# Kernel optimization log

Measured on AMD Instinct MI355X. Metric: run time of the kernel, lower is better.

The kernel has to match this reference:

```python
import jax, jax.numpy as jnp
import numpy as np

B, T, D = 1024, 512, 64   # batch, seq_len, input_dim
H, L, OUT = 8, 3, 1       # hidden (mid_dim), num_layers, output_dim


def setup_inputs() -> dict:
    key = jax.random.key(0)
    ks = jax.random.split(key, 18)
    s = 1.0 / np.sqrt(H)  # torch LSTM default init scale
    u = lambda k, shape: jax.random.uniform(k, shape, jnp.float32, -s, s)
    return {
        "input_seq": jax.random.normal(ks[0], (B, T, D), jnp.float32),
        "h0": jax.random.normal(ks[1], (L, B, H), jnp.float32),
        "c0": jax.random.normal(ks[2], (L, B, H), jnp.float32),
        # encoder LSTM params (layer0 input dim differs)
        "enc_Wih0": u(ks[3], (4 * H, D)),
        "enc_Wih_rest": u(ks[4], (L - 1, 4 * H, H)),
        "enc_Whh": u(ks[5], (L, 4 * H, H)),
        "enc_bih": u(ks[6], (L, 4 * H)),
        "enc_bhh": u(ks[7], (L, 4 * H)),
        # decoder LSTM params
        "dec_Wih0": u(ks[8], (4 * H, D)),
        "dec_Wih_rest": u(ks[9], (L - 1, 4 * H, H)),
        "dec_Whh": u(ks[10], (L, 4 * H, H)),
        "dec_bih": u(ks[11], (L, 4 * H)),
        "dec_bhh": u(ks[12], (L, 4 * H)),
        # decoder output projection
        "lin_W": u(ks[13], (OUT, H)),
        "lin_b": u(ks[14], (OUT,)),
    }


def _cell(x, h, c, Wih, Whh, b):
    # one LSTM cell step, torch gate order: i, f, g, o
    gates = x @ Wih.T + h @ Whh.T + b  # [B, 4H]
    i, f, g, o = jnp.split(gates, 4, axis=-1)
    c2 = jax.nn.sigmoid(f) * c + jax.nn.sigmoid(i) * jnp.tanh(g)
    h2 = jax.nn.sigmoid(o) * jnp.tanh(c2)
    return h2, c2


def _stack_step(h, c, x_t, Wih0, Wih_rest, Whh, bih, bhh):
    # one timestep through all L layers; h, c: [L, B, H]
    hs, cs = [], []
    inp = x_t
    for l in range(L):
        Wih = Wih0 if l == 0 else Wih_rest[l - 1]
        h_l, c_l = _cell(inp, h[l], c[l], Wih, Whh[l], bih[l] + bhh[l])
        hs.append(h_l)
        cs.append(c_l)
        inp = h_l
    return jnp.stack(hs), jnp.stack(cs)


def reference(input_seq, h0, c0, enc_Wih0, enc_Wih_rest, enc_Whh, enc_bih, enc_bhh,
              dec_Wih0, dec_Wih_rest, dec_Whh, dec_bih, dec_bhh, lin_W, lin_b):
    x_tbd = jnp.transpose(input_seq, (1, 0, 2))  # [T, B, D] for scan

    # Encoder: full-sequence 3-layer LSTM, keep final (h, c)
    def enc_step(carry, x_t):
        h, c = carry
        h2, c2 = _stack_step(h, c, x_t, enc_Wih0, enc_Wih_rest, enc_Whh, enc_bih, enc_bhh)
        return (h2, c2), None

    (h, c), _ = jax.lax.scan(enc_step, (h0, c0), x_tbd)

    # Decoder: one LSTM step per timestep, fed the input at that step
    def dec_step(carry, x_t):
        h, c = carry
        h2, c2 = _stack_step(h, c, x_t, dec_Wih0, dec_Wih_rest, dec_Whh, dec_bih, dec_bhh)
        return (h2, c2), None

    (h, c), _ = jax.lax.scan(dec_step, (h, c), x_tbd)

    # original returns outputs[:, -1, :] = linear applied to last decoder output
    pred_last = h[-1] @ lin_W.T + lin_b  # [B, OUT]
    return pred_last
```

## Files before the change

### kernel.cpp

```cpp
#include <hip/hip_runtime.h>

#define TT 512
#define DD 64
#define BB 1024
#define PF 8
#define HH 8

typedef float v2f __attribute__((ext_vector_type(2)));

__device__ __forceinline__ float fexp2(float x){ return __builtin_amdgcn_exp2f(x); }
__device__ __forceinline__ float frcp (float x){ return __builtin_amdgcn_rcpf(x); }

__device__ __forceinline__ v2f bc2(float s){ v2f r; r.x = s; r.y = s; return r; }

#if defined(__has_builtin)
#if __has_builtin(__builtin_elementwise_fma)
#define HAVE_EW_FMA 1
#endif
#endif

__device__ __forceinline__ v2f vfma(v2f a, v2f b, v2f c){
#ifdef HAVE_EW_FMA
  return __builtin_elementwise_fma(a, b, c);
#else
  v2f r; r.x = fmaf(a.x, b.x, c.x); r.y = fmaf(a.y, b.y, c.y); return r;
#endif
}

template<int C>
__device__ __forceinline__ float dppf(float x){
  return __int_as_float(__builtin_amdgcn_update_dpp(0, __float_as_int(x), C, 0xF, 0xF, true));
}
template<int C>
__device__ __forceinline__ int dppi(int x){
  return __builtin_amdgcn_update_dpp(0, x, C, 0xF, 0xF, true);
}

template<int N> struct IC { static constexpr int v = N; };

__global__ __launch_bounds__(256) void proj_kernel(
    const float* __restrict__ x,
    const float* __restrict__ eWih0, const float* __restrict__ eBih, const float* __restrict__ eBhh,
    const float* __restrict__ dWih0, const float* __restrict__ dBih, const float* __restrict__ dBhh,
    float* __restrict__ P)
{
  __shared__ __align__(16) float xs[4][2][16 * 64];
  const int tid  = threadIdx.x;
  const int w    = tid >> 6;
  const int lane = tid & 63;
  const int ph   = lane >> 5;
  const int r    = lane & 31;
  const float* W = ph ? dWih0 : eWih0;
  const float b0 = ph ? (dBih[r] + dBhh[r]) : (eBih[r] + eBhh[r]);
  const int gate = r >> 3, j = r & 7;
  const int pos  = (gate * 4 + (j & 3)) * 2 + (j >> 2);

  float Wx[64];
#pragma unroll
  for (int k = 0; k < 16; ++k) {
    float4 wq = *(const float4*)(W + r * 64 + k * 4);
    Wx[k*4+0] = wq.x; Wx[k*4+1] = wq.y; Wx[k*4+2] = wq.z; Wx[k*4+3] = wq.w;
  }

  const int base_row = (blockIdx.x * 4 + w) * 64;
  const float* xg = x + (size_t)base_row * 64;

  float4 st[4];
#pragma unroll
  for (int i = 0; i < 4; ++i) st[i] = *(const float4*)(xg + i * 256 + lane * 4);
#pragma unroll
  for (int i = 0; i < 4; ++i) *(float4*)&xs[w][0][i * 256 + lane * 4] = st[i];
#pragma unroll
  for (int i = 0; i < 4; ++i) st[i] = *(const float4*)(xg + 1024 + i * 256 + lane * 4);

#pragma unroll 1
  for (int g = 0; g < 4; ++g) {
    const float* buf = &xs[w][g & 1][0];
#pragma unroll 2
    for (int ri = 0; ri < 16; ++ri) {
      float a0 = b0, a1 = 0.f, a2 = 0.f, a3 = 0.f;
#pragma unroll
      for (int kc = 0; kc < 16; ++kc) {
        float4 xv = *(const float4*)(buf + ri * 64 + kc * 4);
        a0 = fmaf(Wx[kc*4+0], xv.x, a0);
        a1 = fmaf(Wx[kc*4+1], xv.y, a1);
        a2 = fmaf(Wx[kc*4+2], xv.z, a2);
        a3 = fmaf(Wx[kc*4+3], xv.w, a3);
      }
      const int row = base_row + g * 16 + ri;
      const int e = row >> 9, t = row & 511;
      P[((size_t)((ph << 10) + e) * TT + t) * 32 + pos] = (a0 + a1) + (a2 + a3);
    }
    if (g < 3) {
#pragma unroll
      for (int i = 0; i < 4; ++i) *(float4*)&xs[w][(g + 1) & 1][i * 256 + lane * 4] = st[i];
      if (g < 2) {
#pragma unroll
        for (int i = 0; i < 4; ++i)
          st[i] = *(const float4*)(xg + (size_t)(g + 2) * 1024 + i * 256 + lane * 4);
      }
    }
  }
}

__global__ __launch_bounds__(64) void recur_kernel(
    const float* __restrict__ P,
    const float* __restrict__ h0,    const float* __restrict__ c0,
    const float* __restrict__ eWihR, const float* __restrict__ eWhh,
    const float* __restrict__ eBih,  const float* __restrict__ eBhh,
    const float* __restrict__ dWihR, const float* __restrict__ dWhh,
    const float* __restrict__ dBih,  const float* __restrict__ dBhh,
    const float* __restrict__ linW,  const float* __restrict__ linB,
    float* __restrict__ out)
{
  const int lane = threadIdx.x;
  const int row  = lane >> 4;
  const int L    = lane & 15;
  const int u    = L >> 2;
  const int g    = L & 3;
  const int e    = blockIdx.x * 4 + row;

  const bool is_tanh = (g == 2);
  const float ns_act = is_tanh ? -2.885390082f : -1.44269504f;
  const float a_act  = is_tanh ? 2.0f : 1.0f;
  const float b_act  = is_tanh ? -1.0f : 0.0f;

  const int p4 = dppi<0x124>(u);
  const int d  = __builtin_amdgcn_readfirstlane((p4 - u) & 3);

  v2f H[3], cs[3], sd[3];
  v2f bd1 = bc2(0.f), bd2 = bc2(0.f);
  v2f WS[3][8], WB[2][8], Bss[2];

#pragma unroll
  for (int l = 0; l < 3; ++l) {
    H[l].x  = h0[((size_t)l * BB + e) * HH + u];
    H[l].y  = h0[((size_t)l * BB + e) * HH + u + 4];
    cs[l].x = c0[((size_t)l * BB + e) * HH + u];
    cs[l].y = c0[((size_t)l * BB + e) * HH + u + 4];
  }

  auto load_phase = [&](const float* WihR, const float* Whh,
                        const float* Bih, const float* Bhh) {
#pragma unroll
    for (int l = 0; l < 3; ++l) {
      const int r0 = l * 32 + g * 8 + u;
#pragma unroll
      for (int k = 0; k < 4; ++k) {
        const int col = (u + d * k) & 3;
        WS[l][k].x     = Whh[r0 * 8 + col];
        WS[l][k].y     = Whh[(r0 + 4) * 8 + col];
        WS[l][4 + k].x = Whh[r0 * 8 + 4 + col];
        WS[l][4 + k].y = Whh[(r0 + 4) * 8 + 4 + col];
      }
    }
#pragma unroll
    for (int l = 0; l < 2; ++l) {
      const int r0 = l * 32 + g * 8 + u;
#pragma unroll
      for (int k = 0; k < 4; ++k) {
        const int col = (u + d * k) & 3;
        WB[l][k].x     = WihR[r0 * 8 + col];
        WB[l][k].y     = WihR[(r0 + 4) * 8 + col];
        WB[l][4 + k].x = WihR[r0 * 8 + 4 + col];
        WB[l][4 + k].y = WihR[(r0 + 4) * 8 + 4 + col];
      }
      Bss[l].x = Bih[(l + 1) * 32 + g * 8 + u]     + Bhh[(l + 1) * 32 + g * 8 + u];
      Bss[l].y = Bih[(l + 1) * 32 + g * 8 + u + 4] + Bhh[(l + 1) * 32 + g * 8 + u + 4];
    }
#pragma unroll
    for (int l = 0; l < 3; ++l) {
      float A0[4], B0[4];
      A0[0] = H[l].x; A0[1] = dppf<0x124>(H[l].x); A0[2] = dppf<0x128>(H[l].x); A0[3] = dppf<0x12C>(H[l].x);
      B0[0] = H[l].y; B0[1] = dppf<0x124>(H[l].y); B0[2] = dppf<0x128>(H[l].y); B0[3] = dppf<0x12C>(H[l].y);
      v2f acc = bc2(0.f);
      if (l) acc = Bss[l - 1];
#pragma unroll
      for (int k = 0; k < 4; ++k) {
        acc = vfma(WS[l][k],     bc2(A0[k]), acc);
        acc = vfma(WS[l][4 + k], bc2(B0[k]), acc);
      }
      sd[l] = acc;
    }
  };

  auto lstep = [&](auto LC, v2f in) -> v2f {
    constexpr int l = decltype(LC)::v;
    v2f pre = in + sd[l];
    v2f ex; ex.x = fexp2(ns_act * pre.x); ex.y = fexp2(ns_act * pre.y);
    v2f rc; rc.x = frcp(1.f + ex.x);      rc.y = frcp(1.f + ex.y);
    v2f act = vfma(bc2(a_act), rc, bc2(b_act));
    v2f Gi, Gf, Gg, Go;
    Gi.x = dppf<0x00>(act.x); Gi.y = dppf<0x00>(act.y);
    Gf.x = dppf<0x55>(act.x); Gf.y = dppf<0x55>(act.y);
    Gg.x = dppf<0xAA>(act.x); Gg.y = dppf<0xAA>(act.y);
    Go.x = dppf<0xFF>(act.x); Go.y = dppf<0xFF>(act.y);
    v2f cn = vfma(Gf, cs[l], Gi * Gg);
    cs[l] = cn;
    v2f tx; tx.x = fexp2(-2.885390082f * cn.x); tx.y = fexp2(-2.885390082f * cn.y);
    v2f tr; tr.x = frcp(1.f + tx.x);            tr.y = frcp(1.f + tx.y);
    v2f th = vfma(bc2(2.f), tr, bc2(-1.f));
    v2f hn = Go * th;
    H[l] = hn;
    float A0[4], B0[4];
    A0[0] = hn.x; A0[1] = dppf<0x124>(hn.x); A0[2] = dppf<0x128>(hn.x); A0[3] = dppf<0x12C>(hn.x);
    B0[0] = hn.y; B0[1] = dppf<0x124>(hn.y); B0[2] = dppf<0x128>(hn.y); B0[3] = dppf<0x12C>(hn.y);
    v2f accS;
    if constexpr (l > 0) accS = Bss[l - 1]; else accS = bc2(0.f);
    v2f accB = bc2(0.f);
#pragma unroll
    for (int k = 0; k < 4; ++k) {
      accS = vfma(WS[l][k],     bc2(A0[k]), accS);
      accS = vfma(WS[l][4 + k], bc2(B0[k]), accS);
      if constexpr (l < 2) {
        accB = vfma(WB[l][k],     bc2(A0[k]), accB);
        accB = vfma(WB[l][4 + k], bc2(B0[k]), accB);
      }
    }
    sd[l] = accS;
    return accB;
  };

#pragma unroll 1
  for (int ph = 0; ph < 2; ++ph) {
    if (ph == 0) load_phase(eWihR, eWhh, eBih, eBhh);
    else         load_phase(dWihR, dWhh, dBih, dBhh);

    const float* Pb = P + ((size_t)((ph << 10) + e) * TT) * 32 + (g * 4 + u) * 2;

    v2f pf[PF];
#pragma unroll
    for (int k = 0; k < PF; ++k) pf[k] = *(const v2f*)(Pb + k * 32);

#pragma unroll
    for (int k = 0; k < PF; ++k) {
      v2f cur = pf[k];
      pf[k] = *(const v2f*)(Pb + (k + PF) * 32);
      v2f n1 = lstep(IC<0>{}, cur);
      v2f n2 = bc2(0.f);
      if (k >= 1) n2 = lstep(IC<1>{}, bd1);
      if (k >= 2) (void)lstep(IC<2>{}, bd2);
      bd1 = n1; bd2 = n2;
    }

#pragma unroll 1
    for (int t = PF; t < TT; t += PF) {
#pragma unroll
      for (int k = 0; k < PF; ++k) {
        v2f cur = pf[k];
        int tn = t + k + PF; if (tn > TT - 1) tn = TT - 1;
        pf[k] = *(const v2f*)(Pb + tn * 32);
        v2f n1 = lstep(IC<0>{}, cur);
        v2f n2 = lstep(IC<1>{}, bd1);
        (void)lstep(IC<2>{}, bd2);
        bd1 = n1; bd2 = n2;
      }
    }

    v2f dd = lstep(IC<1>{}, bd1);
    (void)lstep(IC<2>{}, bd2);
    (void)lstep(IC<2>{}, dd);
  }

  float lwA[4], lwB[4];
#pragma unroll
  for (int k = 0; k < 4; ++k) {
    const int col = (u + d * k) & 3;
    lwA[k] = linW[col];
    lwB[k] = linW[4 + col];
  }
  float A0[4], B0[4];
  A0[0] = H[2].x; A0[1] = dppf<0x124>(H[2].x); A0[2] = dppf<0x128>(H[2].x); A0[3] = dppf<0x12C>(H[2].x);
  B0[0] = H[2].y; B0[1] = dppf<0x124>(H[2].y); B0[2] = dppf<0x128>(H[2].y); B0[3] = dppf<0x12C>(H[2].y);
  float pred = linB[0];
#pragma unroll
  for (int k = 0; k < 4; ++k) {
    pred = fmaf(lwA[k], A0[k], pred);
    pred = fmaf(lwB[k], B0[k], pred);
  }
  if (L == 0) out[e] = pred;
}

__global__ __launch_bounds__(64) void seq2seq_fallback(
    const float* __restrict__ x, const float* __restrict__ h0, const float* __restrict__ c0,
    const float* __restrict__ eWih0, const float* __restrict__ eWihR, const float* __restrict__ eWhh,
    const float* __restrict__ eBih,  const float* __restrict__ eBhh,
    const float* __restrict__ dWih0, const float* __restrict__ dWihR, const float* __restrict__ dWhh,
    const float* __restrict__ dBih,  const float* __restrict__ dBhh,
    const float* __restrict__ linW,  const float* __restrict__ linB, float* __restrict__ out)
{
  const int tid = threadIdx.x;
  const int g   = tid & 31;
  const int grp = tid & 32;
  const int jj  = g & 7;
  const int e   = blockIdx.x * 2 + (tid >> 5);
  const bool is_tanh = ((g >> 3) == 2);
  const float s_act = is_tanh ? 2.885390082f : 1.44269504f;
  const float a_act = is_tanh ? 2.0f : 1.0f;
  const float b_act = is_tanh ? -1.0f : 0.0f;
  float hrep[3][8]; float cc[3];
#pragma unroll
  for (int l = 0; l < 3; ++l) {
#pragma unroll
    for (int k = 0; k < 8; ++k) hrep[l][k] = h0[((size_t)l * BB + e) * HH + k];
    cc[l] = c0[((size_t)l * BB + e) * HH + jj];
  }
  for (int p = 0; p < 2; ++p) {
    const float* Wih0 = p ? dWih0 : eWih0;  const float* WihR = p ? dWihR : eWihR;
    const float* Whh  = p ? dWhh  : eWhh;   const float* Bih  = p ? dBih  : eBih;
    const float* Bhh  = p ? dBhh  : eBhh;
    float Wx[64];
#pragma unroll
    for (int k = 0; k < 64; k += 4) {
      float4 w = *(const float4*)(Wih0 + g * 64 + k);
      Wx[k] = w.x; Wx[k+1] = w.y; Wx[k+2] = w.z; Wx[k+3] = w.w;
    }
    float Wh[3][8], Wi[2][8], bias[3];
#pragma unroll
    for (int l = 0; l < 3; ++l) {
#pragma unroll
      for (int k = 0; k < 8; ++k) Wh[l][k] = Whh[(l*32+g)*8+k];
      bias[l] = Bih[l*32+g] + Bhh[l*32+g];
    }
#pragma unroll
    for (int l = 0; l < 2; ++l)
#pragma unroll
      for (int k = 0; k < 8; ++k) Wi[l][k] = WihR[(l*32+g)*8+k];
    const float* xrow = x + (size_t)e * TT * DD;
    for (int t = 0; t < TT; ++t) {
      float4 acc = make_float4(bias[0], 0.f, 0.f, 0.f);
#pragma unroll
      for (int kc = 0; kc < 16; ++kc) {
        float4 xv = *(const float4*)(xrow + kc * 4);
        acc.x = fmaf(Wx[kc*4+0], xv.x, acc.x); acc.y = fmaf(Wx[kc*4+1], xv.y, acc.y);
        acc.z = fmaf(Wx[kc*4+2], xv.z, acc.z); acc.w = fmaf(Wx[kc*4+3], xv.w, acc.w);
      }
      float pre = (acc.x + acc.y) + (acc.z + acc.w);
      { float r0=0.f,r1=0.f;
#pragma unroll
        for (int k = 0; k < 8; k += 2) { r0=fmaf(Wh[0][k],hrep[0][k],r0); r1=fmaf(Wh[0][k+1],hrep[0][k+1],r1); }
        pre += r0 + r1; }
#pragma unroll
      for (int l = 0; l < 3; ++l) {
        if (l > 0) {
          float r0 = bias[l], r1 = 0.f;
#pragma unroll
          for (int k = 0; k < 8; k += 2) {
            r0=fmaf(Wi[l-1][k],hrep[l-1][k],r0); r1=fmaf(Wi[l-1][k+1],hrep[l-1][k+1],r1);
            r0=fmaf(Wh[l][k],hrep[l][k],r0);     r1=fmaf(Wh[l][k+1],hrep[l][k+1],r1);
          }
          pre = r0 + r1;
        }
        float act = fmaf(a_act, frcp(1.0f + fexp2(-s_act * pre)), b_act);
        float iv = __shfl(act, grp + jj);
        float fv = __shfl(act, grp + 8 + jj);
        float gv = __shfl(act, grp + 16 + jj);
        float ov = __shfl(act, grp + 24 + jj);
        float cn = fmaf(fv, cc[l], iv * gv);
        cc[l] = cn;
        float th = fmaf(2.0f, frcp(1.0f + fexp2(-2.885390082f * cn)), -1.0f);
        float hn = ov * th;
#pragma unroll
        for (int k = 0; k < 8; ++k) hrep[l][k] = __shfl(hn, grp + k);
      }
      xrow += DD;
    }
  }
  float pred = linB[0];
#pragma unroll
  for (int k = 0; k < 8; ++k) pred = fmaf(linW[k], hrep[2][k], pred);
  if (g == 0) out[e] = pred;
}

extern "C" void kernel_launch(void* const* d_in, const int* in_sizes, int n_in,
                              void* d_out, int out_size, void* d_ws, size_t ws_size,
                              hipStream_t stream) {
  const float* x     = (const float*)d_in[0];
  const float* h0    = (const float*)d_in[1];
  const float* c0    = (const float*)d_in[2];
  const float* eWih0 = (const float*)d_in[3];
  const float* eWihR = (const float*)d_in[4];
  const float* eWhh  = (const float*)d_in[5];
  const float* eBih  = (const float*)d_in[6];
  const float* eBhh  = (const float*)d_in[7];
  const float* dWih0 = (const float*)d_in[8];
  const float* dWihR = (const float*)d_in[9];
  const float* dWhh  = (const float*)d_in[10];
  const float* dBih  = (const float*)d_in[11];
  const float* dBhh  = (const float*)d_in[12];
  const float* linW  = (const float*)d_in[13];
  const float* linB  = (const float*)d_in[14];
  float* out = (float*)d_out;

  const size_t P_BYTES = (size_t)2 * BB * TT * 32 * sizeof(float);
  if (ws_size >= P_BYTES) {
    float* P = (float*)d_ws;
    proj_kernel<<<2048, 256, 0, stream>>>(x, eWih0, eBih, eBhh, dWih0, dBih, dBhh, P);
    recur_kernel<<<BB / 4, 64, 0, stream>>>(P, h0, c0, eWihR, eWhh, eBih, eBhh,
                                            dWihR, dWhh, dBih, dBhh, linW, linB, out);
  } else {
    seq2seq_fallback<<<BB / 2, 64, 0, stream>>>(x, h0, c0, eWih0, eWihR, eWhh, eBih, eBhh,
                                                dWih0, dWihR, dWhh, dBih, dBhh, linW, linB, out);
  }
}
```

Baseline: 644.8 us.

## Split LSTM layers across three wavefronts with LDS handoff pipeline

```diff
diff --git a/kernel.cpp b/kernel.cpp
--- a/kernel.cpp
+++ b/kernel.cpp
@@ -35,8 +35,6 @@
 __device__ __forceinline__ int dppi(int x){
   return __builtin_amdgcn_update_dpp(0, x, C, 0xF, 0xF, true);
 }
-
-template<int N> struct IC { static constexpr int v = N; };
 
 __global__ __launch_bounds__(256) void proj_kernel(
     const float* __restrict__ x,
@@ -103,7 +101,7 @@
   }
 }
 
-__global__ __launch_bounds__(64) void recur_kernel(
+__global__ __launch_bounds__(192) void recur_kernel(
     const float* __restrict__ P,
     const float* __restrict__ h0,    const float* __restrict__ c0,
     const float* __restrict__ eWihR, const float* __restrict__ eWhh,
@@ -113,7 +111,12 @@
     const float* __restrict__ linW,  const float* __restrict__ linB,
     float* __restrict__ out)
 {
-  const int lane = threadIdx.x;
+  __shared__ v2f bufA[2][64];
+  __shared__ v2f bufB[2][64];
+
+  const int tid  = threadIdx.x;
+  const int w    = tid >> 6;
+  const int lane = tid & 63;
   const int row  = lane >> 4;
   const int L    = lane & 15;
   const int u    = L >> 2;
@@ -125,68 +128,59 @@
   const float a_act  = is_tanh ? 2.0f : 1.0f;
   const float b_act  = is_tanh ? -1.0f : 0.0f;
 
+  const bool seedb = (w > 0);
+  const bool below = (w < 2);
+
   const int p4 = dppi<0x124>(u);
   const int d  = __builtin_amdgcn_readfirstlane((p4 - u) & 3);
 
-  v2f H[3], cs[3], sd[3];
-  v2f bd1 = bc2(0.f), bd2 = bc2(0.f);
-  v2f WS[3][8], WB[2][8], Bss[2];
-
-#pragma unroll
-  for (int l = 0; l < 3; ++l) {
-    H[l].x  = h0[((size_t)l * BB + e) * HH + u];
-    H[l].y  = h0[((size_t)l * BB + e) * HH + u + 4];
-    cs[l].x = c0[((size_t)l * BB + e) * HH + u];
-    cs[l].y = c0[((size_t)l * BB + e) * HH + u + 4];
-  }
+  v2f Hm, cm, sdm;
+  v2f WSm[8], WBm[8], Bsm = bc2(0.f);
+
+  Hm.x = h0[((size_t)w * BB + e) * HH + u];
+  Hm.y = h0[((size_t)w * BB + e) * HH + u + 4];
+  cm.x = c0[((size_t)w * BB + e) * HH + u];
+  cm.y = c0[((size_t)w * BB + e) * HH + u + 4];
 
   auto load_phase = [&](const float* WihR, const float* Whh,
                         const float* Bih, const float* Bhh) {
-#pragma unroll
-    for (int l = 0; l < 3; ++l) {
-      const int r0 = l * 32 + g * 8 + u;
+    const int r0 = w * 32 + g * 8 + u;
+#pragma unroll
+    for (int k = 0; k < 4; ++k) {
+      const int col = (u + d * k) & 3;
+      WSm[k].x     = Whh[r0 * 8 + col];
+      WSm[k].y     = Whh[(r0 + 4) * 8 + col];
+      WSm[4 + k].x = Whh[r0 * 8 + 4 + col];
+      WSm[4 + k].y = Whh[(r0 + 4) * 8 + 4 + col];
+    }
+    if (below) {
 #pragma unroll
       for (int k = 0; k < 4; ++k) {
         const int col = (u + d * k) & 3;
-        WS[l][k].x     = Whh[r0 * 8 + col];
-        WS[l][k].y     = Whh[(r0 + 4) * 8 + col];
-        WS[l][4 + k].x = Whh[r0 * 8 + 4 + col];
-        WS[l][4 + k].y = Whh[(r0 + 4) * 8 + 4 + col];
-      }
-    }
-#pragma unroll
-    for (int l = 0; l < 2; ++l) {
-      const int r0 = l * 32 + g * 8 + u;
-#pragma unroll
-      for (int k = 0; k < 4; ++k) {
-        const int col = (u + d * k) & 3;
-        WB[l][k].x     = WihR[r0 * 8 + col];
-        WB[l][k].y     = WihR[(r0 + 4) * 8 + col];
-        WB[l][4 + k].x = WihR[r0 * 8 + 4 + col];
-        WB[l][4 + k].y = WihR[(r0 + 4) * 8 + 4 + col];
-      }
-      Bss[l].x = Bih[(l + 1) * 32 + g * 8 + u]     + Bhh[(l + 1) * 32 + g * 8 + u];
-      Bss[l].y = Bih[(l + 1) * 32 + g * 8 + u + 4] + Bhh[(l + 1) * 32 + g * 8 + u + 4];
-    }
-#pragma unroll
-    for (int l = 0; l < 3; ++l) {
-      float A0[4], B0[4];
-      A0[0] = H[l].x; A0[1] = dppf<0x124>(H[l].x); A0[2] = dppf<0x128>(H[l].x); A0[3] = dppf<0x12C>(H[l].x);
-      B0[0] = H[l].y; B0[1] = dppf<0x124>(H[l].y); B0[2] = dppf<0x128>(H[l].y); B0[3] = dppf<0x12C>(H[l].y);
-      v2f acc = bc2(0.f);
-      if (l) acc = Bss[l - 1];
-#pragma unroll
-      for (int k = 0; k < 4; ++k) {
-        acc = vfma(WS[l][k],     bc2(A0[k]), acc);
-        acc = vfma(WS[l][4 + k], bc2(B0[k]), acc);
-      }
-      sd[l] = acc;
-    }
+        WBm[k].x     = WihR[r0 * 8 + col];
+        WBm[k].y     = WihR[(r0 + 4) * 8 + col];
+        WBm[4 + k].x = WihR[r0 * 8 + 4 + col];
+        WBm[4 + k].y = WihR[(r0 + 4) * 8 + 4 + col];
+      }
+    }
+    if (seedb) {
+      Bsm.x = Bih[w * 32 + g * 8 + u]     + Bhh[w * 32 + g * 8 + u];
+      Bsm.y = Bih[w * 32 + g * 8 + u + 4] + Bhh[w * 32 + g * 8 + u + 4];
+    }
+    float A0[4], B0[4];
+    A0[0] = Hm.x; A0[1] = dppf<0x124>(Hm.x); A0[2] = dppf<0x128>(Hm.x); A0[3] = dppf<0x12C>(Hm.x);
+    B0[0] = Hm.y; B0[1] = dppf<0x124>(Hm.y); B0[2] = dppf<0x128>(Hm.y); B0[3] = dppf<0x12C>(Hm.y);
+    v2f acc = seedb ? Bsm : bc2(0.f);
+#pragma unroll
+    for (int k = 0; k < 4; ++k) {
+      acc = vfma(WSm[k],     bc2(A0[k]), acc);
+      acc = vfma(WSm[4 + k], bc2(B0[k]), acc);
+    }
+    sdm = acc;
   };
 
-  auto lstep = [&](auto LC, v2f in) -> v2f {
-    constexpr int l = decltype(LC)::v;
-    v2f pre = in + sd[l];
+  auto lstep = [&](v2f in) -> v2f {
+    v2f pre = in + sdm;
     v2f ex; ex.x = fexp2(ns_act * pre.x); ex.y = fexp2(ns_act * pre.y);
     v2f rc; rc.x = frcp(1.f + ex.x);      rc.y = frcp(1.f + ex.y);
     v2f act = vfma(bc2(a_act), rc, bc2(b_act));
@@ -195,29 +189,31 @@
     Gf.x = dppf<0x55>(act.x); Gf.y = dppf<0x55>(act.y);
     Gg.x = dppf<0xAA>(act.x); Gg.y = dppf<0xAA>(act.y);
     Go.x = dppf<0xFF>(act.x); Go.y = dppf<0xFF>(act.y);
-    v2f cn = vfma(Gf, cs[l], Gi * Gg);
-    cs[l] = cn;
+    v2f cn = vfma(Gf, cm, Gi * Gg);
+    cm = cn;
     v2f tx; tx.x = fexp2(-2.885390082f * cn.x); tx.y = fexp2(-2.885390082f * cn.y);
     v2f tr; tr.x = frcp(1.f + tx.x);            tr.y = frcp(1.f + tx.y);
     v2f th = vfma(bc2(2.f), tr, bc2(-1.f));
     v2f hn = Go * th;
-    H[l] = hn;
+    Hm = hn;
     float A0[4], B0[4];
     A0[0] = hn.x; A0[1] = dppf<0x124>(hn.x); A0[2] = dppf<0x128>(hn.x); A0[3] = dppf<0x12C>(hn.x);
     B0[0] = hn.y; B0[1] = dppf<0x124>(hn.y); B0[2] = dppf<0x128>(hn.y); B0[3] = dppf<0x12C>(hn.y);
-    v2f accS;
-    if constexpr (l > 0) accS = Bss[l - 1]; else accS = bc2(0.f);
+    v2f accS = seedb ? Bsm : bc2(0.f);
+#pragma unroll
+    for (int k = 0; k < 4; ++k) {
+      accS = vfma(WSm[k],     bc2(A0[k]), accS);
+      accS = vfma(WSm[4 + k], bc2(B0[k]), accS);
+    }
+    sdm = accS;
     v2f accB = bc2(0.f);
-#pragma unroll
-    for (int k = 0; k < 4; ++k) {
-      accS = vfma(WS[l][k],     bc2(A0[k]), accS);
-      accS = vfma(WS[l][4 + k], bc2(B0[k]), accS);
-      if constexpr (l < 2) {
-        accB = vfma(WB[l][k],     bc2(A0[k]), accB);
-        accB = vfma(WB[l][4 + k], bc2(B0[k]), accB);
-      }
-    }
-    sd[l] = accS;
+    if (below) {
+#pragma unroll
+      for (int k = 0; k < 4; ++k) {
+        accB = vfma(WBm[k],     bc2(A0[k]), accB);
+        accB = vfma(WBm[4 + k], bc2(B0[k]), accB);
+      }
+    }
     return accB;
   };
 
@@ -229,56 +225,72 @@
     const float* Pb = P + ((size_t)((ph << 10) + e) * TT) * 32 + (g * 4 + u) * 2;
 
     v2f pf[PF];
-#pragma unroll
-    for (int k = 0; k < PF; ++k) pf[k] = *(const v2f*)(Pb + k * 32);
-
-#pragma unroll
-    for (int k = 0; k < PF; ++k) {
-      v2f cur = pf[k];
-      pf[k] = *(const v2f*)(Pb + (k + PF) * 32);
-      v2f n1 = lstep(IC<0>{}, cur);
-      v2f n2 = bc2(0.f);
-      if (k >= 1) n2 = lstep(IC<1>{}, bd1);
-      if (k >= 2) (void)lstep(IC<2>{}, bd2);
-      bd1 = n1; bd2 = n2;
+    if (w == 0) {
+#pragma unroll
+      for (int k = 0; k < PF; ++k) pf[k] = *(const v2f*)(Pb + k * 32);
     }
 
 #pragma unroll 1
-    for (int t = PF; t < TT; t += PF) {
-#pragma unroll
-      for (int k = 0; k < PF; ++k) {
-        v2f cur = pf[k];
-        int tn = t + k + PF; if (tn > TT - 1) tn = TT - 1;
-        pf[k] = *(const v2f*)(Pb + tn * 32);
-        v2f n1 = lstep(IC<0>{}, cur);
-        v2f n2 = lstep(IC<1>{}, bd1);
-        (void)lstep(IC<2>{}, bd2);
-        bd1 = n1; bd2 = n2;
-      }
-    }
-
-    v2f dd = lstep(IC<1>{}, bd1);
-    (void)lstep(IC<2>{}, bd2);
-    (void)lstep(IC<2>{}, dd);
-  }
-
-  float lwA[4], lwB[4];
-#pragma unroll
-  for (int k = 0; k < 4; ++k) {
-    const int col = (u + d * k) & 3;
-    lwA[k] = linW[col];
-    lwB[k] = linW[4 + col];
-  }
-  float A0[4], B0[4];
-  A0[0] = H[2].x; A0[1] = dppf<0x124>(H[2].x); A0[2] = dppf<0x128>(H[2].x); A0[3] = dppf<0x12C>(H[2].x);
-  B0[0] = H[2].y; B0[1] = dppf<0x124>(H[2].y); B0[2] = dppf<0x128>(H[2].y); B0[3] = dppf<0x12C>(H[2].y);
-  float pred = linB[0];
-#pragma unroll
-  for (int k = 0; k < 4; ++k) {
-    pred = fmaf(lwA[k], A0[k], pred);
-    pred = fmaf(lwB[k], B0[k], pred);
-  }
-  if (L == 0) out[e] = pred;
+    for (int kb = 0; kb < TT; kb += PF) {
+#pragma unroll
+      for (int j = 0; j < PF; ++j) {
+        const int k = kb + j;
+        if (w == 0) {
+          v2f cur = pf[j];
+          int tn = k + PF; if (tn > TT - 1) tn = TT - 1;
+          pf[j] = *(const v2f*)(Pb + tn * 32);
+          v2f n1 = lstep(cur);
+          bufA[j & 1][lane] = n1;
+        } else if (w == 1) {
+          if (k >= 1) {
+            v2f i1 = bufA[(j ^ 1) & 1][lane];
+            v2f n2 = lstep(i1);
+            bufB[(j ^ 1) & 1][lane] = n2;
+          }
+        } else {
+          if (k >= 2) {
+            v2f i2 = bufB[j & 1][lane];
+            (void)lstep(i2);
+          }
+        }
+        __syncthreads();
+      }
+    }
+    if (w == 1) {
+      v2f i1 = bufA[1][lane];
+      v2f n2 = lstep(i1);
+      bufB[1][lane] = n2;
+    } else if (w == 2) {
+      v2f i2 = bufB[0][lane];
+      (void)lstep(i2);
+    }
+    __syncthreads();
+    if (w == 2) {
+      v2f i2 = bufB[1][lane];
+      (void)lstep(i2);
+    }
+    __syncthreads();
+  }
+
+  if (w == 2) {
+    float lwA[4], lwB[4];
+#pragma unroll
+    for (int k = 0; k < 4; ++k) {
+      const int col = (u + d * k) & 3;
+      lwA[k] = linW[col];
+      lwB[k] = linW[4 + col];
+    }
+    float A0[4], B0[4];
+    A0[0] = Hm.x; A0[1] = dppf<0x124>(Hm.x); A0[2] = dppf<0x128>(Hm.x); A0[3] = dppf<0x12C>(Hm.x);
+    B0[0] = Hm.y; B0[1] = dppf<0x124>(Hm.y); B0[2] = dppf<0x128>(Hm.y); B0[3] = dppf<0x12C>(Hm.y);
+    float pred = linB[0];
+#pragma unroll
+    for (int k = 0; k < 4; ++k) {
+      pred = fmaf(lwA[k], A0[k], pred);
+      pred = fmaf(lwB[k], B0[k], pred);
+    }
+    if (L == 0) out[e] = pred;
+  }
 }
 
 __global__ __launch_bounds__(64) void seq2seq_fallback(
@@ -396,8 +408,8 @@
   if (ws_size >= P_BYTES) {
     float* P = (float*)d_ws;
     proj_kernel<<<2048, 256, 0, stream>>>(x, eWih0, eBih, eBhh, dWih0, dBih, dBhh, P);
-    recur_kernel<<<BB / 4, 64, 0, stream>>>(P, h0, c0, eWihR, eWhh, eBih, eBhh,
-                                            dWihR, dWhh, dBih, dBhh, linW, linB, out);
+    recur_kernel<<<BB / 4, 192, 0, stream>>>(P, h0, c0, eWihR, eWhh, eBih, eBhh,
+                                             dWihR, dWhh, dBih, dBhh, linW, linB, out);
   } else {
     seq2seq_fallback<<<BB / 2, 64, 0, stream>>>(x, h0, c0, eWih0, eWihR, eWhh, eBih, eBhh,
                                                 dWih0, dWihR, dWhh, dBih, dBhh, linW, linB, out);
```

New measurement: 651.8 us. No clear change (+1.1%).

## Spread recurrence over 32 lanes per sequence, one hidden unit per lane

Applied to the files above, without the earlier changes.

```diff
diff --git a/kernel.cpp b/kernel.cpp
--- a/kernel.cpp
+++ b/kernel.cpp
@@ -11,22 +11,6 @@
 __device__ __forceinline__ float fexp2(float x){ return __builtin_amdgcn_exp2f(x); }
 __device__ __forceinline__ float frcp (float x){ return __builtin_amdgcn_rcpf(x); }
 
-__device__ __forceinline__ v2f bc2(float s){ v2f r; r.x = s; r.y = s; return r; }
-
-#if defined(__has_builtin)
-#if __has_builtin(__builtin_elementwise_fma)
-#define HAVE_EW_FMA 1
-#endif
-#endif
-
-__device__ __forceinline__ v2f vfma(v2f a, v2f b, v2f c){
-#ifdef HAVE_EW_FMA
-  return __builtin_elementwise_fma(a, b, c);
-#else
-  v2f r; r.x = fmaf(a.x, b.x, c.x); r.y = fmaf(a.y, b.y, c.y); return r;
-#endif
-}
-
 template<int C>
 __device__ __forceinline__ float dppf(float x){
   return __int_as_float(__builtin_amdgcn_update_dpp(0, __float_as_int(x), C, 0xF, 0xF, true));
@@ -34,6 +18,10 @@
 template<int C>
 __device__ __forceinline__ int dppi(int x){
   return __builtin_amdgcn_update_dpp(0, x, C, 0xF, 0xF, true);
+}
+
+__device__ __forceinline__ float swz16(float x){
+  return __int_as_float(__builtin_amdgcn_ds_swizzle(__float_as_int(x), 0x401F));
 }
 
 template<int N> struct IC { static constexpr int v = N; };
@@ -103,7 +91,7 @@
   }
 }
 
-__global__ __launch_bounds__(64) void recur_kernel(
+__global__ __launch_bounds__(128) void recur_kernel(
     const float* __restrict__ P,
     const float* __restrict__ h0,    const float* __restrict__ c0,
     const float* __restrict__ eWihR, const float* __restrict__ eWhh,
@@ -113,111 +101,113 @@
     const float* __restrict__ linW,  const float* __restrict__ linB,
     float* __restrict__ out)
 {
-  const int lane = threadIdx.x;
-  const int row  = lane >> 4;
-  const int L    = lane & 15;
-  const int u    = L >> 2;
-  const int g    = L & 3;
-  const int e    = blockIdx.x * 4 + row;
+  const int tid = threadIdx.x;
+  const int idx = tid & 31;
+  const int v   = idx >> 2;
+  const int g   = idx & 3;
+  const int b   = v & 3;
+  const bool rB = (v >= 4);
+  const int e   = blockIdx.x * 4 + (tid >> 5);
 
   const bool is_tanh = (g == 2);
   const float ns_act = is_tanh ? -2.885390082f : -1.44269504f;
   const float a_act  = is_tanh ? 2.0f : 1.0f;
   const float b_act  = is_tanh ? -1.0f : 0.0f;
 
-  const int p4 = dppi<0x124>(u);
-  const int d  = __builtin_amdgcn_readfirstlane((p4 - u) & 3);
-
-  v2f H[3], cs[3], sd[3];
-  v2f bd1 = bc2(0.f), bd2 = bc2(0.f);
-  v2f WS[3][8], WB[2][8], Bss[2];
+  const int qidx = (tid >> 2) & 3;
+  const int p4 = dppi<0x124>(qidx);
+  const int d  = __builtin_amdgcn_readfirstlane((p4 - qidx) & 3);
+
+  float H[3], cs[3], sd[3];
+  float bd1 = 0.f, bd2 = 0.f;
+  float WS[3][8], WB[2][8], Bss[2];
 
 #pragma unroll
   for (int l = 0; l < 3; ++l) {
-    H[l].x  = h0[((size_t)l * BB + e) * HH + u];
-    H[l].y  = h0[((size_t)l * BB + e) * HH + u + 4];
-    cs[l].x = c0[((size_t)l * BB + e) * HH + u];
-    cs[l].y = c0[((size_t)l * BB + e) * HH + u + 4];
-  }
+    H[l]  = h0[((size_t)l * BB + e) * HH + v];
+    cs[l] = c0[((size_t)l * BB + e) * HH + v];
+  }
+
+  auto bcast = [&](float hn, float* A, float* Bv) {
+    float Hsw = swz16(hn);
+    float Lo = rB ? Hsw : hn;
+    float Hi = rB ? hn : Hsw;
+    A[0]  = Lo; A[1]  = dppf<0x124>(Lo); A[2]  = dppf<0x128>(Lo); A[3]  = dppf<0x12C>(Lo);
+    Bv[0] = Hi; Bv[1] = dppf<0x124>(Hi); Bv[2] = dppf<0x128>(Hi); Bv[3] = dppf<0x12C>(Hi);
+  };
 
   auto load_phase = [&](const float* WihR, const float* Whh,
                         const float* Bih, const float* Bhh) {
 #pragma unroll
     for (int l = 0; l < 3; ++l) {
-      const int r0 = l * 32 + g * 8 + u;
+      const int r0 = l * 32 + g * 8 + v;
 #pragma unroll
       for (int k = 0; k < 4; ++k) {
-        const int col = (u + d * k) & 3;
-        WS[l][k].x     = Whh[r0 * 8 + col];
-        WS[l][k].y     = Whh[(r0 + 4) * 8 + col];
-        WS[l][4 + k].x = Whh[r0 * 8 + 4 + col];
-        WS[l][4 + k].y = Whh[(r0 + 4) * 8 + 4 + col];
+        const int col = (b + d * k) & 3;
+        WS[l][k]     = Whh[r0 * 8 + col];
+        WS[l][4 + k] = Whh[r0 * 8 + 4 + col];
       }
     }
 #pragma unroll
     for (int l = 0; l < 2; ++l) {
-      const int r0 = l * 32 + g * 8 + u;
+      const int r0 = l * 32 + g * 8 + v;
 #pragma unroll
       for (int k = 0; k < 4; ++k) {
-        const int col = (u + d * k) & 3;
-        WB[l][k].x     = WihR[r0 * 8 + col];
-        WB[l][k].y     = WihR[(r0 + 4) * 8 + col];
-        WB[l][4 + k].x = WihR[r0 * 8 + 4 + col];
-        WB[l][4 + k].y = WihR[(r0 + 4) * 8 + 4 + col];
-      }
-      Bss[l].x = Bih[(l + 1) * 32 + g * 8 + u]     + Bhh[(l + 1) * 32 + g * 8 + u];
-      Bss[l].y = Bih[(l + 1) * 32 + g * 8 + u + 4] + Bhh[(l + 1) * 32 + g * 8 + u + 4];
+        const int col = (b + d * k) & 3;
+        WB[l][k]     = WihR[r0 * 8 + col];
+        WB[l][4 + k] = WihR[r0 * 8 + 4 + col];
+      }
+      Bss[l] = Bih[(l + 1) * 32 + g * 8 + v] + Bhh[(l + 1) * 32 + g * 8 + v];
     }
 #pragma unroll
     for (int l = 0; l < 3; ++l) {
-      float A0[4], B0[4];
-      A0[0] = H[l].x; A0[1] = dppf<0x124>(H[l].x); A0[2] = dppf<0x128>(H[l].x); A0[3] = dppf<0x12C>(H[l].x);
-      B0[0] = H[l].y; B0[1] = dppf<0x124>(H[l].y); B0[2] = dppf<0x128>(H[l].y); B0[3] = dppf<0x12C>(H[l].y);
-      v2f acc = bc2(0.f);
-      if (l) acc = Bss[l - 1];
+      float A[4], Bv[4];
+      bcast(H[l], A, Bv);
+      float acc = l ? Bss[l - 1] : 0.f;
 #pragma unroll
       for (int k = 0; k < 4; ++k) {
-        acc = vfma(WS[l][k],     bc2(A0[k]), acc);
-        acc = vfma(WS[l][4 + k], bc2(B0[k]), acc);
+        acc = fmaf(WS[l][k],     A[k],  acc);
+        acc = fmaf(WS[l][4 + k], Bv[k], acc);
       }
       sd[l] = acc;
     }
   };
 
-  auto lstep = [&](auto LC, v2f in) -> v2f {
+  auto lstep = [&](auto LC, float in) -> float {
     constexpr int l = decltype(LC)::v;
-    v2f pre = in + sd[l];
-    v2f ex; ex.x = fexp2(ns_act * pre.x); ex.y = fexp2(ns_act * pre.y);
-    v2f rc; rc.x = frcp(1.f + ex.x);      rc.y = frcp(1.f + ex.y);
-    v2f act = vfma(bc2(a_act), rc, bc2(b_act));
-    v2f Gi, Gf, Gg, Go;
-    Gi.x = dppf<0x00>(act.x); Gi.y = dppf<0x00>(act.y);
-    Gf.x = dppf<0x55>(act.x); Gf.y = dppf<0x55>(act.y);
-    Gg.x = dppf<0xAA>(act.x); Gg.y = dppf<0xAA>(act.y);
-    Go.x = dppf<0xFF>(act.x); Go.y = dppf<0xFF>(act.y);
-    v2f cn = vfma(Gf, cs[l], Gi * Gg);
+    float pre = in + sd[l];
+    float ex  = fexp2(ns_act * pre);
+    float rc  = frcp(1.f + ex);
+    float act = fmaf(a_act, rc, b_act);
+    float Gi = dppf<0x00>(act);
+    float Gf = dppf<0x55>(act);
+    float Gg = dppf<0xAA>(act);
+    float Go = dppf<0xFF>(act);
+    float cn = fmaf(Gf, cs[l], Gi * Gg);
     cs[l] = cn;
-    v2f tx; tx.x = fexp2(-2.885390082f * cn.x); tx.y = fexp2(-2.885390082f * cn.y);
-    v2f tr; tr.x = frcp(1.f + tx.x);            tr.y = frcp(1.f + tx.y);
-    v2f th = vfma(bc2(2.f), tr, bc2(-1.f));
-    v2f hn = Go * th;
+    float tx = fexp2(-2.885390082f * cn);
+    float tr = frcp(1.f + tx);
+    float th = fmaf(2.f, tr, -1.f);
+    float hn = Go * th;
     H[l] = hn;
-    float A0[4], B0[4];
-    A0[0] = hn.x; A0[1] = dppf<0x124>(hn.x); A0[2] = dppf<0x128>(hn.x); A0[3] = dppf<0x12C>(hn.x);
-    B0[0] = hn.y; B0[1] = dppf<0x124>(hn.y); B0[2] = dppf<0x128>(hn.y); B0[3] = dppf<0x12C>(hn.y);
-    v2f accS;
-    if constexpr (l > 0) accS = Bss[l - 1]; else accS = bc2(0.f);
-    v2f accB = bc2(0.f);
+    float A[4], Bv[4];
+    bcast(hn, A, Bv);
+    float accS;
+    if constexpr (l > 0) accS = Bss[l - 1]; else accS = 0.f;
 #pragma unroll
     for (int k = 0; k < 4; ++k) {
-      accS = vfma(WS[l][k],     bc2(A0[k]), accS);
-      accS = vfma(WS[l][4 + k], bc2(B0[k]), accS);
-      if constexpr (l < 2) {
-        accB = vfma(WB[l][k],     bc2(A0[k]), accB);
-        accB = vfma(WB[l][4 + k], bc2(B0[k]), accB);
-      }
+      accS = fmaf(WS[l][k],     A[k],  accS);
+      accS = fmaf(WS[l][4 + k], Bv[k], accS);
     }
     sd[l] = accS;
+    float accB = 0.f;
+    if constexpr (l < 2) {
+#pragma unroll
+      for (int k = 0; k < 4; ++k) {
+        accB = fmaf(WB[l][k],     A[k],  accB);
+        accB = fmaf(WB[l][4 + k], Bv[k], accB);
+      }
+    }
     return accB;
   };
 
@@ -226,18 +216,19 @@
     if (ph == 0) load_phase(eWihR, eWhh, eBih, eBhh);
     else         load_phase(dWihR, dWhh, dBih, dBhh);
 
-    const float* Pb = P + ((size_t)((ph << 10) + e) * TT) * 32 + (g * 4 + u) * 2;
-
-    v2f pf[PF];
-#pragma unroll
-    for (int k = 0; k < PF; ++k) pf[k] = *(const v2f*)(Pb + k * 32);
+    const int pos = (g * 4 + b) * 2 + (v >> 2);
+    const float* Pb = P + ((size_t)((ph << 10) + e) * TT) * 32 + pos;
+
+    float pf[PF];
+#pragma unroll
+    for (int k = 0; k < PF; ++k) pf[k] = Pb[k * 32];
 
 #pragma unroll
     for (int k = 0; k < PF; ++k) {
-      v2f cur = pf[k];
-      pf[k] = *(const v2f*)(Pb + (k + PF) * 32);
-      v2f n1 = lstep(IC<0>{}, cur);
-      v2f n2 = bc2(0.f);
+      float cur = pf[k];
+      pf[k] = Pb[(k + PF) * 32];
+      float n1 = lstep(IC<0>{}, cur);
+      float n2 = 0.f;
       if (k >= 1) n2 = lstep(IC<1>{}, bd1);
       if (k >= 2) (void)lstep(IC<2>{}, bd2);
       bd1 = n1; bd2 = n2;
@@ -247,17 +238,17 @@
     for (int t = PF; t < TT; t += PF) {
 #pragma unroll
       for (int k = 0; k < PF; ++k) {
-        v2f cur = pf[k];
+        float cur = pf[k];
         int tn = t + k + PF; if (tn > TT - 1) tn = TT - 1;
-        pf[k] = *(const v2f*)(Pb + tn * 32);
-        v2f n1 = lstep(IC<0>{}, cur);
-        v2f n2 = lstep(IC<1>{}, bd1);
+        pf[k] = Pb[(size_t)tn * 32];
+        float n1 = lstep(IC<0>{}, cur);
+        float n2 = lstep(IC<1>{}, bd1);
         (void)lstep(IC<2>{}, bd2);
         bd1 = n1; bd2 = n2;
       }
     }
 
-    v2f dd = lstep(IC<1>{}, bd1);
+    float dd = lstep(IC<1>{}, bd1);
     (void)lstep(IC<2>{}, bd2);
     (void)lstep(IC<2>{}, dd);
   }
@@ -265,20 +256,19 @@
   float lwA[4], lwB[4];
 #pragma unroll
   for (int k = 0; k < 4; ++k) {
-    const int col = (u + d * k) & 3;
+    const int col = (b + d * k) & 3;
     lwA[k] = linW[col];
     lwB[k] = linW[4 + col];
   }
-  float A0[4], B0[4];
-  A0[0] = H[2].x; A0[1] = dppf<0x124>(H[2].x); A0[2] = dppf<0x128>(H[2].x); A0[3] = dppf<0x12C>(H[2].x);
-  B0[0] = H[2].y; B0[1] = dppf<0x124>(H[2].y); B0[2] = dppf<0x128>(H[2].y); B0[3] = dppf<0x12C>(H[2].y);
+  float A[4], Bv[4];
+  bcast(H[2], A, Bv);
   float pred = linB[0];
 #pragma unroll
   for (int k = 0; k < 4; ++k) {
-    pred = fmaf(lwA[k], A0[k], pred);
-    pred = fmaf(lwB[k], B0[k], pred);
-  }
-  if (L == 0) out[e] = pred;
+    pred = fmaf(lwA[k], A[k],  pred);
+    pred = fmaf(lwB[k], Bv[k], pred);
+  }
+  if (idx == 0) out[e] = pred;
 }
 
 __global__ __launch_bounds__(64) void seq2seq_fallback(
@@ -396,8 +386,8 @@
   if (ws_size >= P_BYTES) {
     float* P = (float*)d_ws;
     proj_kernel<<<2048, 256, 0, stream>>>(x, eWih0, eBih, eBhh, dWih0, dBih, dBhh, P);
-    recur_kernel<<<BB / 4, 64, 0, stream>>>(P, h0, c0, eWihR, eWhh, eBih, eBhh,
-                                            dWihR, dWhh, dBih, dBhh, linW, linB, out);
+    recur_kernel<<<BB / 4, 128, 0, stream>>>(P, h0, c0, eWihR, eWhh, eBih, eBhh,
+                                             dWihR, dWhh, dBih, dBhh, linW, linB, out);
   } else {
     seq2seq_fallback<<<BB / 2, 64, 0, stream>>>(x, h0, c0, eWih0, eWihR, eWhh, eBih, eBhh,
                                                 dWih0, dWihR, dWhh, dBih, dBhh, linW, linB, out);
```

New measurement: 607.1 us. 5.8% less time.
